# Performance work log

Hardware: AMD Instinct MI355X
Metric: run time of the kernel (lower is better)

Reference implementation:

```python
import jax, jax.numpy as jnp
import numpy as np
import math

B, H, S, D = 8, 16, 1024, 64

def setup_inputs() -> dict:
    key = jax.random.key(0)
    kq, kk, kv, km = jax.random.split(key, 4)
    queries = jax.random.normal(kq, (B, H, S, D), dtype=jnp.float32)
    keys = jax.random.normal(kk, (B, H, S, D), dtype=jnp.float32)
    values = jax.random.normal(kv, (B, H, S, D), dtype=jnp.float32)
    mask = jax.random.randint(km, (B, 1, S, S), 0, 2, dtype=jnp.int32)
    return {"queries": queries, "keys": keys, "values": values, "mask": mask}

def reference(queries, keys, values, mask):
    d = values.shape[3]
    # scores: [B,H,S,S] = Q @ K^T / sqrt(d)
    scores = jnp.einsum('bhqd,bhkd->bhqk', queries, keys) / math.sqrt(d)
    attn = jax.nn.softmax(scores, axis=-1)
    # Faithful to source: mask applied AFTER softmax via masked_fill(mask==0, -100000)
    attn = jnp.where(mask == 0, jnp.float32(-100000.0), attn)
    out = jnp.einsum('bhqk,bhkd->bhqd', attn, values)
    return (out, attn)
```

## Files before the change

### kernel.cpp

```cpp
#include <hip/hip_runtime.h>

constexpr int Bm = 8, Hm = 16, Sm = 1024, Dm = 64;
constexpr int BH = Bm * Hm;
constexpr int NBLK = BH * (Sm / 16);
constexpr int STRIDE = 1040;

typedef short short8  __attribute__((ext_vector_type(8)));
typedef float floatx4 __attribute__((ext_vector_type(4)));
typedef int   intx4   __attribute__((ext_vector_type(4)));

__device__ inline unsigned short f2bf(float f) {
    unsigned u = __builtin_bit_cast(unsigned, f);
    u += 0x7fffu + ((u >> 16) & 1u);
    return (unsigned short)(u >> 16);
}
__device__ inline float bf2f(unsigned short h) {
    unsigned u = ((unsigned)h) << 16;
    return __builtin_bit_cast(float, u);
}

__global__ __launch_bounds__(256)
void preconv(const float* __restrict__ K, const float* __restrict__ V,
             unsigned short* __restrict__ Kbf, unsigned short* __restrict__ VT)
{
    __shared__ unsigned short tile[64][72];

    const int blk = blockIdx.x;
    const int bh  = blk >> 4;
    const int t   = blk & 15;
    const int tid = threadIdx.x;
    const int row = tid >> 2;
    const int c0  = (tid & 3) << 4;

    {
        const float* src = K + ((size_t)bh * Sm + t * 64 + row) * Dm + c0;
        unsigned short* dst = Kbf + ((size_t)bh * Sm + t * 64 + row) * Dm + c0;
        floatx4 a0 = *(const floatx4*)(src);
        floatx4 a1 = *(const floatx4*)(src + 4);
        floatx4 a2 = *(const floatx4*)(src + 8);
        floatx4 a3 = *(const floatx4*)(src + 12);
        short8 p0, p1;
        #pragma unroll
        for (int i = 0; i < 4; ++i) {
            p0[i]     = (short)f2bf(a0[i]);
            p0[i + 4] = (short)f2bf(a1[i]);
            p1[i]     = (short)f2bf(a2[i]);
            p1[i + 4] = (short)f2bf(a3[i]);
        }
        *(short8*)(dst)     = p0;
        *(short8*)(dst + 8) = p1;
    }

    {
        const float* src = V + ((size_t)bh * Sm + t * 64 + row) * Dm + c0;
        floatx4 a0 = *(const floatx4*)(src);
        floatx4 a1 = *(const floatx4*)(src + 4);
        floatx4 a2 = *(const floatx4*)(src + 8);
        floatx4 a3 = *(const floatx4*)(src + 12);
        short8 p0, p1;
        #pragma unroll
        for (int i = 0; i < 4; ++i) {
            p0[i]     = (short)f2bf(a0[i]);
            p0[i + 4] = (short)f2bf(a1[i]);
            p1[i]     = (short)f2bf(a2[i]);
            p1[i + 4] = (short)f2bf(a3[i]);
        }
        *(short8*)(&tile[row][c0])     = p0;
        *(short8*)(&tile[row][c0 + 8]) = p1;
    }
    __syncthreads();
    {
        const int drow = tid >> 2;
        const int kc0  = (tid & 3) << 4;
        unsigned short* dst = VT + ((size_t)bh * Dm + drow) * Sm + t * 64 + kc0;
        short8 p0, p1;
        #pragma unroll
        for (int j = 0; j < 8; ++j) {
            p0[j] = (short)tile[kc0 + j][drow];
            p1[j] = (short)tile[kc0 + 8 + j][drow];
        }
        *(short8*)(dst)     = p0;
        *(short8*)(dst + 8) = p1;
    }
}

__global__ __launch_bounds__(256, 4)
void attn_fused(const float* __restrict__ Q, const unsigned short* __restrict__ Kbf,
                const unsigned short* __restrict__ VT, const int* __restrict__ Msk,
                float* __restrict__ Out, float* __restrict__ Attn)
{
    __shared__ __align__(16) unsigned short strip[16 * STRIDE];

    const int tid  = threadIdx.x;
    const int wave = tid >> 6;
    const int lane = tid & 63;
    const int quad = lane >> 4;
    const int ln   = lane & 15;

    const int bid = (blockIdx.x & 7) * (NBLK >> 3) + (blockIdx.x >> 3);
    const int bh = bid >> 6;
    const int qt = bid & 63;
    const int q0 = qt << 4;
    const int b  = bh >> 4;

    const float* Qb = Q + (size_t)bh * (Sm * Dm);
    const unsigned short* Kb = Kbf + (size_t)bh * (Sm * Dm);
    const unsigned short* Vb = VT + (size_t)bh * (Dm * Sm);

    short8 aq0, aq1;
    {
        const float* qrow = Qb + (q0 + ln) * Dm + quad * 8;
        floatx4 a = *(const floatx4*)(qrow);
        floatx4 c = *(const floatx4*)(qrow + 4);
        floatx4 d = *(const floatx4*)(qrow + 32);
        floatx4 e = *(const floatx4*)(qrow + 36);
        #pragma unroll
        for (int i = 0; i < 4; ++i) {
            aq0[i]     = (short)f2bf(a[i] * 0.125f);
            aq0[i + 4] = (short)f2bf(c[i] * 0.125f);
            aq1[i]     = (short)f2bf(d[i] * 0.125f);
            aq1[i + 4] = (short)f2bf(e[i] * 0.125f);
        }
    }

    for (int kt = wave * 16; kt < wave * 16 + 16; ++kt) {
        const unsigned short* krow = Kb + (kt * 16 + ln) * Dm + quad * 8;
        short8 b0 = *(const short8*)(krow);
        short8 b1 = *(const short8*)(krow + 32);
        floatx4 c = {0.f, 0.f, 0.f, 0.f};
        c = __builtin_amdgcn_mfma_f32_16x16x32_bf16(aq0, b0, c, 0, 0, 0);
        c = __builtin_amdgcn_mfma_f32_16x16x32_bf16(aq1, b1, c, 0, 0, 0);
        const int colb = kt * 16 + ln;
        #pragma unroll
        for (int r = 0; r < 4; ++r)
            strip[(quad * 4 + r) * STRIDE + colb] = f2bf(c[r]);
    }
    __syncthreads();

    {
        const int row = tid >> 4, l = tid & 15;
        unsigned short* srow = strip + row * STRIDE;

        float mx = -1e30f;
        #pragma unroll
        for (int i = 0; i < 8; ++i) {
            short8 v = *(const short8*)(srow + l * 8 + i * 128);
            #pragma unroll
            for (int j = 0; j < 8; ++j) mx = fmaxf(mx, bf2f((unsigned short)v[j]));
        }
        #pragma unroll
        for (int off = 8; off >= 1; off >>= 1) mx = fmaxf(mx, __shfl_xor(mx, off, 16));

        float sum = 0.f;
        #pragma unroll
        for (int i = 0; i < 8; ++i) {
            short8 v = *(const short8*)(srow + l * 8 + i * 128);
            short8 e;
            #pragma unroll
            for (int j = 0; j < 8; ++j) {
                float x = __expf(bf2f((unsigned short)v[j]) - mx);
                sum += x;
                e[j] = (short)f2bf(x);
            }
            *(short8*)(srow + l * 8 + i * 128) = e;
        }
        #pragma unroll
        for (int off = 8; off >= 1; off >>= 1) sum += __shfl_xor(sum, off, 16);
        const float rn = 1.f / sum;

        const int* mrow  = Msk + (size_t)b * (Sm * Sm) + (size_t)(q0 + row) * Sm;
        float*     arow  = Attn + ((size_t)bh * Sm + (q0 + row)) * Sm;
        #pragma unroll
        for (int i = 0; i < 8; ++i) {
            const int c0 = l * 8 + i * 128;
            short8 v  = *(const short8*)(srow + c0);
            intx4  m0 = *(const intx4*)(mrow + c0);
            intx4  m1 = *(const intx4*)(mrow + c0 + 4);
            float p[8];
            #pragma unroll
            for (int j = 0; j < 4; ++j) {
                p[j]     = (m0[j] != 0) ? bf2f((unsigned short)v[j])     * rn : -100000.f;
                p[j + 4] = (m1[j] != 0) ? bf2f((unsigned short)v[j + 4]) * rn : -100000.f;
            }
            floatx4 o0, o1;
            short8 pf;
            #pragma unroll
            for (int j = 0; j < 4; ++j) { o0[j] = p[j]; o1[j] = p[j + 4]; }
            #pragma unroll
            for (int j = 0; j < 8; ++j) pf[j] = (short)f2bf(p[j]);
            *(short8*)(srow + c0) = pf;
            *(floatx4*)(arow + c0)     = o0;
            *(floatx4*)(arow + c0 + 4) = o1;
        }
    }
    __syncthreads();

    floatx4 acc[4] = {{0,0,0,0},{0,0,0,0},{0,0,0,0},{0,0,0,0}};
    for (int kb = wave * 256; kb < wave * 256 + 256; kb += 32) {
        short8 af = *(const short8*)(strip + ln * STRIDE + kb + quad * 8);
        const unsigned short* vbase = Vb + kb + quad * 8;
        #pragma unroll
        for (int n0 = 0; n0 < 4; ++n0) {
            short8 bf = *(const short8*)(vbase + (size_t)(n0 * 16 + ln) * Sm);
            acc[n0] = __builtin_amdgcn_mfma_f32_16x16x32_bf16(af, bf, acc[n0], 0, 0, 0);
        }
    }
    __syncthreads();

    float* part = (float*)strip;
    #pragma unroll
    for (int n0 = 0; n0 < 4; ++n0)
        #pragma unroll
        for (int r = 0; r < 4; ++r)
            part[wave * 1024 + (quad * 4 + r) * 64 + n0 * 16 + ln] = acc[n0][r];
    __syncthreads();
    {
        const int o4 = tid * 4;
        floatx4 s = *(const floatx4*)(part + o4);
        s += *(const floatx4*)(part + 1024 + o4);
        s += *(const floatx4*)(part + 2048 + o4);
        s += *(const floatx4*)(part + 3072 + o4);
        const int row = o4 >> 6, dc = o4 & 63;
        *(floatx4*)(Out + (size_t)bh * (Sm * Dm) + (size_t)(q0 + row) * Dm + dc) = s;
    }
}

__global__ __launch_bounds__(256, 4)
void attn_fused_f32(const float* __restrict__ Q, const float* __restrict__ K,
                    const float* __restrict__ V, const int* __restrict__ Msk,
                    float* __restrict__ Out, float* __restrict__ Attn)
{
    __shared__ __align__(16) unsigned short strip[16 * STRIDE];

    const int tid  = threadIdx.x;
    const int wave = tid >> 6;
    const int lane = tid & 63;
    const int quad = lane >> 4;
    const int ln   = lane & 15;

    const int bid = (blockIdx.x & 7) * (NBLK >> 3) + (blockIdx.x >> 3);
    const int bh = bid >> 6;
    const int qt = bid & 63;
    const int q0 = qt << 4;
    const int b  = bh >> 4;

    const float* Qb = Q + (size_t)bh * (Sm * Dm);
    const float* Kb = K + (size_t)bh * (Sm * Dm);
    const float* Vb = V + (size_t)bh * (Sm * Dm);

    short8 aq0, aq1;
    {
        const float* qrow = Qb + (q0 + ln) * Dm + quad * 8;
        floatx4 a = *(const floatx4*)(qrow);
        floatx4 c = *(const floatx4*)(qrow + 4);
        floatx4 d = *(const floatx4*)(qrow + 32);
        floatx4 e = *(const floatx4*)(qrow + 36);
        #pragma unroll
        for (int i = 0; i < 4; ++i) {
            aq0[i]     = (short)f2bf(a[i] * 0.125f);
            aq0[i + 4] = (short)f2bf(c[i] * 0.125f);
            aq1[i]     = (short)f2bf(d[i] * 0.125f);
            aq1[i + 4] = (short)f2bf(e[i] * 0.125f);
        }
    }

    for (int kt = wave * 16; kt < wave * 16 + 16; ++kt) {
        const float* krow = Kb + (kt * 16 + ln) * Dm + quad * 8;
        floatx4 k0 = *(const floatx4*)(krow);
        floatx4 k1 = *(const floatx4*)(krow + 4);
        floatx4 k2 = *(const floatx4*)(krow + 32);
        floatx4 k3 = *(const floatx4*)(krow + 36);
        short8 b0, b1;
        #pragma unroll
        for (int i = 0; i < 4; ++i) {
            b0[i]     = (short)f2bf(k0[i]);
            b0[i + 4] = (short)f2bf(k1[i]);
            b1[i]     = (short)f2bf(k2[i]);
            b1[i + 4] = (short)f2bf(k3[i]);
        }
        floatx4 c = {0.f, 0.f, 0.f, 0.f};
        c = __builtin_amdgcn_mfma_f32_16x16x32_bf16(aq0, b0, c, 0, 0, 0);
        c = __builtin_amdgcn_mfma_f32_16x16x32_bf16(aq1, b1, c, 0, 0, 0);
        const int colb = kt * 16 + ln;
        #pragma unroll
        for (int r = 0; r < 4; ++r)
            strip[(quad * 4 + r) * STRIDE + colb] = f2bf(c[r]);
    }
    __syncthreads();

    {
        const int row = tid >> 4, l = tid & 15;
        unsigned short* srow = strip + row * STRIDE;

        float mx = -1e30f;
        #pragma unroll
        for (int i = 0; i < 8; ++i) {
            short8 v = *(const short8*)(srow + l * 8 + i * 128);
            #pragma unroll
            for (int j = 0; j < 8; ++j) mx = fmaxf(mx, bf2f((unsigned short)v[j]));
        }
        #pragma unroll
        for (int off = 8; off >= 1; off >>= 1) mx = fmaxf(mx, __shfl_xor(mx, off, 16));

        float sum = 0.f;
        #pragma unroll
        for (int i = 0; i < 8; ++i) {
            short8 v = *(const short8*)(srow + l * 8 + i * 128);
            short8 e;
            #pragma unroll
            for (int j = 0; j < 8; ++j) {
                float x = __expf(bf2f((unsigned short)v[j]) - mx);
                sum += x;
                e[j] = (short)f2bf(x);
            }
            *(short8*)(srow + l * 8 + i * 128) = e;
        }
        #pragma unroll
        for (int off = 8; off >= 1; off >>= 1) sum += __shfl_xor(sum, off, 16);
        const float rn = 1.f / sum;

        const int* mrow  = Msk + (size_t)b * (Sm * Sm) + (size_t)(q0 + row) * Sm;
        float*     arow  = Attn + ((size_t)bh * Sm + (q0 + row)) * Sm;
        #pragma unroll
        for (int i = 0; i < 8; ++i) {
            const int c0 = l * 8 + i * 128;
            short8 v  = *(const short8*)(srow + c0);
            intx4  m0 = *(const intx4*)(mrow + c0);
            intx4  m1 = *(const intx4*)(mrow + c0 + 4);
            float p[8];
            #pragma unroll
            for (int j = 0; j < 4; ++j) {
                p[j]     = (m0[j] != 0) ? bf2f((unsigned short)v[j])     * rn : -100000.f;
                p[j + 4] = (m1[j] != 0) ? bf2f((unsigned short)v[j + 4]) * rn : -100000.f;
            }
            floatx4 o0, o1;
            short8 pf;
            #pragma unroll
            for (int j = 0; j < 4; ++j) { o0[j] = p[j]; o1[j] = p[j + 4]; }
            #pragma unroll
            for (int j = 0; j < 8; ++j) pf[j] = (short)f2bf(p[j]);
            *(short8*)(srow + c0) = pf;
            *(floatx4*)(arow + c0)     = o0;
            *(floatx4*)(arow + c0 + 4) = o1;
        }
    }
    __syncthreads();

    floatx4 acc[4] = {{0,0,0,0},{0,0,0,0},{0,0,0,0},{0,0,0,0}};
    for (int kb = wave * 256; kb < wave * 256 + 256; kb += 32) {
        short8 af = *(const short8*)(strip + ln * STRIDE + kb + quad * 8);
        const float* vbase = Vb + (kb + quad * 8) * Dm + ln;
        #pragma unroll
        for (int n0 = 0; n0 < 4; ++n0) {
            short8 bf;
            #pragma unroll
            for (int j = 0; j < 8; ++j)
                bf[j] = (short)f2bf(vbase[j * Dm + n0 * 16]);
            acc[n0] = __builtin_amdgcn_mfma_f32_16x16x32_bf16(af, bf, acc[n0], 0, 0, 0);
        }
    }
    __syncthreads();

    float* part = (float*)strip;
    #pragma unroll
    for (int n0 = 0; n0 < 4; ++n0)
        #pragma unroll
        for (int r = 0; r < 4; ++r)
            part[wave * 1024 + (quad * 4 + r) * 64 + n0 * 16 + ln] = acc[n0][r];
    __syncthreads();
    {
        const int o4 = tid * 4;
        floatx4 s = *(const floatx4*)(part + o4);
        s += *(const floatx4*)(part + 1024 + o4);
        s += *(const floatx4*)(part + 2048 + o4);
        s += *(const floatx4*)(part + 3072 + o4);
        const int row = o4 >> 6, dc = o4 & 63;
        *(floatx4*)(Out + (size_t)bh * (Sm * Dm) + (size_t)(q0 + row) * Dm + dc) = s;
    }
}

extern "C" void kernel_launch(void* const* d_in, const int* in_sizes, int n_in,
                              void* d_out, int out_size, void* d_ws, size_t ws_size,
                              hipStream_t stream)
{
    const float* Q   = (const float*)d_in[0];
    const float* K   = (const float*)d_in[1];
    const float* V   = (const float*)d_in[2];
    const int*   Msk = (const int*)d_in[3];
    float* Out  = (float*)d_out;
    float* Attn = Out + (size_t)Bm * Hm * Sm * Dm;

    const size_t nElem = (size_t)BH * Sm * Dm;
    const size_t need  = nElem * 2 * sizeof(unsigned short);

    if (d_ws != nullptr && ws_size >= need) {
        unsigned short* Kbf = (unsigned short*)d_ws;
        unsigned short* VT  = Kbf + nElem;
        preconv<<<dim3(BH * 16), dim3(256), 0, stream>>>(K, V, Kbf, VT);
        attn_fused<<<dim3(NBLK), dim3(256), 0, stream>>>(Q, Kbf, VT, Msk, Out, Attn);
    } else {
        attn_fused_f32<<<dim3(NBLK), dim3(256), 0, stream>>>(Q, K, V, Msk, Out, Attn);
    }
}
```

Before: 882.6 us.

## Swizzle score strip in LDS, fuse row max into QK, raise occupancy

Replaces the padded LDS score strip (stride 1040) with an unpadded 1024-wide strip using XOR swizzling, cutting LDS use per block so the launch bound can rise from 4 to 5 blocks. Row maxima are computed in registers during the QK MFMA loop, reduced by shuffle, and handed between waves through a global workspace buffer. This removes the separate max pass over LDS. The cost is extra global writes and reads of the per-wave maxima, plus possible register pressure from the higher occupancy target.

```diff
diff --git a/kernel.cpp b/kernel.cpp
--- a/kernel.cpp
+++ b/kernel.cpp
@@ -3,7 +3,6 @@
 constexpr int Bm = 8, Hm = 16, Sm = 1024, Dm = 64;
 constexpr int BH = Bm * Hm;
 constexpr int NBLK = BH * (Sm / 16);
-constexpr int STRIDE = 1040;
 
 typedef short short8  __attribute__((ext_vector_type(8)));
 typedef float floatx4 __attribute__((ext_vector_type(4)));
@@ -50,7 +49,6 @@
         *(short8*)(dst)     = p0;
         *(short8*)(dst + 8) = p1;
     }
-
     {
         const float* src = V + ((size_t)bh * Sm + t * 64 + row) * Dm + c0;
         floatx4 a0 = *(const floatx4*)(src);
@@ -84,12 +82,13 @@
     }
 }
 
-__global__ __launch_bounds__(256, 4)
+__global__ __launch_bounds__(256, 5)
 void attn_fused(const float* __restrict__ Q, const unsigned short* __restrict__ Kbf,
                 const unsigned short* __restrict__ VT, const int* __restrict__ Msk,
+                float* __restrict__ Gmx,
                 float* __restrict__ Out, float* __restrict__ Attn)
 {
-    __shared__ __align__(16) unsigned short strip[16 * STRIDE];
+    __shared__ __align__(16) unsigned short strip[16 * 1024];
 
     const int tid  = threadIdx.x;
     const int wave = tid >> 6;
@@ -123,6 +122,7 @@
         }
     }
 
+    float rm[4] = {-1e30f, -1e30f, -1e30f, -1e30f};
     for (int kt = wave * 16; kt < wave * 16 + 16; ++kt) {
         const unsigned short* krow = Kb + (kt * 16 + ln) * Dm + quad * 8;
         short8 b0 = *(const short8*)(krow);
@@ -132,29 +132,37 @@
         c = __builtin_amdgcn_mfma_f32_16x16x32_bf16(aq1, b1, c, 0, 0, 0);
         const int colb = kt * 16 + ln;
         #pragma unroll
+        for (int r = 0; r < 4; ++r) {
+            const int row = quad * 4 + r;
+            rm[r] = fmaxf(rm[r], c[r]);
+            strip[row * 1024 + (colb ^ ((row & 7) << 3))] = f2bf(c[r]);
+        }
+    }
+    #pragma unroll
+    for (int off = 8; off >= 1; off >>= 1)
+        #pragma unroll
         for (int r = 0; r < 4; ++r)
-            strip[(quad * 4 + r) * STRIDE + colb] = f2bf(c[r]);
+            rm[r] = fmaxf(rm[r], __shfl_xor(rm[r], off, 16));
+    if (ln == 0) {
+        float* g = Gmx + ((size_t)bid << 6) + wave * 16 + quad * 4;
+        g[0] = rm[0]; g[1] = rm[1]; g[2] = rm[2]; g[3] = rm[3];
     }
     __syncthreads();
 
     {
         const int row = tid >> 4, l = tid & 15;
-        unsigned short* srow = strip + row * STRIDE;
-
-        float mx = -1e30f;
+        const int sw  = (row & 7) << 3;
+        unsigned short* srow = strip + row * 1024;
+
+        const float* g = Gmx + ((size_t)bid << 6) + row;
+        float mx = fmaxf(fmaxf(g[0], g[16]), fmaxf(g[32], g[48]));
+        mx = bf2f(f2bf(mx));
+
+        float sum = 0.f;
         #pragma unroll
         for (int i = 0; i < 8; ++i) {
-            short8 v = *(const short8*)(srow + l * 8 + i * 128);
-            #pragma unroll
-            for (int j = 0; j < 8; ++j) mx = fmaxf(mx, bf2f((unsigned short)v[j]));
-        }
-        #pragma unroll
-        for (int off = 8; off >= 1; off >>= 1) mx = fmaxf(mx, __shfl_xor(mx, off, 16));
-
-        float sum = 0.f;
-        #pragma unroll
-        for (int i = 0; i < 8; ++i) {
-            short8 v = *(const short8*)(srow + l * 8 + i * 128);
+            unsigned short* p8 = srow + ((l * 8 + i * 128) ^ sw);
+            short8 v = *(const short8*)p8;
             short8 e;
             #pragma unroll
             for (int j = 0; j < 8; ++j) {
@@ -162,7 +170,7 @@
                 sum += x;
                 e[j] = (short)f2bf(x);
             }
-            *(short8*)(srow + l * 8 + i * 128) = e;
+            *(short8*)p8 = e;
         }
         #pragma unroll
         for (int off = 8; off >= 1; off >>= 1) sum += __shfl_xor(sum, off, 16);
@@ -173,7 +181,8 @@
         #pragma unroll
         for (int i = 0; i < 8; ++i) {
             const int c0 = l * 8 + i * 128;
-            short8 v  = *(const short8*)(srow + c0);
+            unsigned short* p8 = srow + (c0 ^ sw);
+            short8 v  = *(const short8*)p8;
             intx4  m0 = *(const intx4*)(mrow + c0);
             intx4  m1 = *(const intx4*)(mrow + c0 + 4);
             float p[8];
@@ -188,7 +197,7 @@
             for (int j = 0; j < 4; ++j) { o0[j] = p[j]; o1[j] = p[j + 4]; }
             #pragma unroll
             for (int j = 0; j < 8; ++j) pf[j] = (short)f2bf(p[j]);
-            *(short8*)(srow + c0) = pf;
+            *(short8*)p8 = pf;
             *(floatx4*)(arow + c0)     = o0;
             *(floatx4*)(arow + c0 + 4) = o1;
         }
@@ -197,7 +206,7 @@
 
     floatx4 acc[4] = {{0,0,0,0},{0,0,0,0},{0,0,0,0},{0,0,0,0}};
     for (int kb = wave * 256; kb < wave * 256 + 256; kb += 32) {
-        short8 af = *(const short8*)(strip + ln * STRIDE + kb + quad * 8);
+        short8 af = *(const short8*)(strip + ln * 1024 + ((kb + quad * 8) ^ ((ln & 7) << 3)));
         const unsigned short* vbase = Vb + kb + quad * 8;
         #pragma unroll
         for (int n0 = 0; n0 < 4; ++n0) {
@@ -230,6 +239,7 @@
                     const float* __restrict__ V, const int* __restrict__ Msk,
                     float* __restrict__ Out, float* __restrict__ Attn)
 {
+    constexpr int STRIDE = 1040;
     __shared__ __align__(16) unsigned short strip[16 * STRIDE];
 
     const int tid  = threadIdx.x;
@@ -391,13 +401,16 @@
     float* Attn = Out + (size_t)Bm * Hm * Sm * Dm;
 
     const size_t nElem = (size_t)BH * Sm * Dm;
-    const size_t need  = nElem * 2 * sizeof(unsigned short);
+    const size_t bfBytes = nElem * 2 * sizeof(unsigned short);
+    const size_t gmxBytes = (size_t)NBLK * 64 * sizeof(float);
+    const size_t need = bfBytes + gmxBytes;
 
     if (d_ws != nullptr && ws_size >= need) {
         unsigned short* Kbf = (unsigned short*)d_ws;
         unsigned short* VT  = Kbf + nElem;
+        float*          Gmx = (float*)(VT + nElem);
         preconv<<<dim3(BH * 16), dim3(256), 0, stream>>>(K, V, Kbf, VT);
-        attn_fused<<<dim3(NBLK), dim3(256), 0, stream>>>(Q, Kbf, VT, Msk, Out, Attn);
+        attn_fused<<<dim3(NBLK), dim3(256), 0, stream>>>(Q, Kbf, VT, Msk, Gmx, Out, Attn);
     } else {
         attn_fused_f32<<<dim3(NBLK), dim3(256), 0, stream>>>(Q, K, V, Msk, Out, Attn);
     }
```

Measured after the change: 882.8 us. Within noise of the previous version (+0.0%).
